# Performance work log

Hardware: AMD Instinct MI355X
Metric: run time of the kernel (lower is better)

The kernel has to match this reference:

```python
import jax, jax.numpy as jnp
import numpy as np

B, N, D, H = 8, 1024, 768, 12
HD = D // H
SCALE = HD ** -0.5

def setup_inputs() -> dict:
    key = jax.random.key(0)
    k1, k2, k3, k4 = jax.random.split(key, 4)
    x = jax.random.normal(k1, (B, N, D), dtype=jnp.float32)
    weight = jax.random.uniform(k2, (B, N), dtype=jnp.float32)
    W_qkv = jax.random.normal(k3, (D, 3 * D), dtype=jnp.float32) * (D ** -0.5)
    W_msa = jax.random.normal(k4, (D, D), dtype=jnp.float32) * (D ** -0.5)
    b_msa = jnp.zeros((D,), dtype=jnp.float32)
    return {"x": x, "weight": weight, "W_qkv": W_qkv, "W_msa": W_msa, "b_msa": b_msa}

def reference(x, weight, W_qkv, W_msa, b_msa):
    # QKV projection (no bias), then elementwise per-token gate
    qkv = jnp.einsum('bnd,de->bne', x, W_qkv)          # [B,N,3D]
    qkv = weight[:, :, None] * qkv
    qkv = qkv.reshape(B, N, 3, H, HD).transpose(2, 0, 3, 1, 4)  # [3,B,H,N,hd]
    q, k, v = qkv[0], qkv[1], qkv[2]
    A = jnp.einsum('bhnd,bhmd->bhnm', q, k) * SCALE    # [B,H,N,N]
    A = jax.nn.softmax(A, axis=-1)
    out = jnp.einsum('bhnm,bhmd->bhnd', A, v)          # [B,H,N,hd]
    out = out.transpose(0, 2, 1, 3).reshape(B, N, D)
    return jnp.einsum('bnd,de->bne', out, W_msa) + b_msa
```

## Files before the change

### kernel.cpp

```cpp
#include <hip/hip_runtime.h>
#include <hip/hip_bf16.h>


typedef __attribute__((ext_vector_type(8))) short bf8;
typedef __attribute__((ext_vector_type(4))) float f4;

#define QSCALE 0.1803368801111204f

static __device__ __forceinline__ short bf16_of(float f) {
    union { float f; unsigned u; } a; a.f = f;
    unsigned r = a.u + 0x7FFFu + ((a.u >> 16) & 1u);
    return (short)(r >> 16);
}

static __device__ __forceinline__ unsigned bfpk(float lo, float hi) {
    float2 t; t.x = lo; t.y = hi;
    __hip_bfloat162 b = __float22bfloat162_rn(t);
    union { __hip_bfloat162 b; unsigned u; } c; c.b = b;
    return c.u;
}

static __device__ __forceinline__ void async16(const short* g, short* l) {
    __builtin_amdgcn_global_load_lds(
        (const __attribute__((address_space(1))) void*)g,
        (__attribute__((address_space(3))) void*)l, 16, 0, 0);
}

static __device__ __forceinline__ void transpose64(
        const float* __restrict__ w, short* __restrict__ wt,
        int K, int E, int k0, int e0, int tid, short (*t)[65]) {
#pragma unroll
    for (int p = 0; p < 16; ++p) {
        int idx = p * 256 + tid;
        int r = idx >> 6, c = idx & 63;
        t[r][c] = bf16_of(w[(k0 + r) * E + e0 + c]);
    }
    __syncthreads();
#pragma unroll
    for (int p = 0; p < 16; ++p) {
        int idx = p * 256 + tid;
        int r = idx >> 6, c = idx & 63;
        wt[(e0 + r) * K + k0 + c] = t[c][r];
    }
}

__global__ __launch_bounds__(256) void k_prep(
        const float* __restrict__ x, const float* __restrict__ gate,
        short* __restrict__ xb,
        const float* __restrict__ Wqkv, short* __restrict__ wtq,
        const float* __restrict__ Wmsa, short* __restrict__ wtm) {
    __shared__ short t[64][65];
    const int bid = blockIdx.x, tid = threadIdx.x;
    if (bid < 3072) {
        int i = bid * 256 + tid;
        const float g = gate[i / 96];
        const f4* sp = (const f4*)x;
        f4 a = sp[2 * i], b = sp[2 * i + 1];
        union { bf8 v; short h[8]; } o;
        o.h[0] = bf16_of(a[0] * g); o.h[1] = bf16_of(a[1] * g);
        o.h[2] = bf16_of(a[2] * g); o.h[3] = bf16_of(a[3] * g);
        o.h[4] = bf16_of(b[0] * g); o.h[5] = bf16_of(b[1] * g);
        o.h[6] = bf16_of(b[2] * g); o.h[7] = bf16_of(b[3] * g);
        ((bf8*)xb)[i] = o.v;
    } else if (bid < 3504) {
        int tt = bid - 3072;
        transpose64(Wqkv, wtq, 768, 2304, (tt / 36) * 64, (tt % 36) * 64, tid, t);
    } else {
        int tt = bid - 3504;
        transpose64(Wmsa, wtm, 768, 768, (tt / 12) * 64, (tt % 12) * 64, tid, t);
    }
}

static __device__ __forceinline__ void gemm128(const short* __restrict__ gA,
                                               const short* __restrict__ gB,
                                               short* smem,
                                               f4 acc[4][4]) {
    const int tid = threadIdx.x, lane = tid & 63;
    const int l16 = lane & 15, quad = lane >> 4, rx = l16 & 7;
    const int wm = (tid >> 6) & 1, wn = tid >> 7;

    auto stage = [&](short* S, int k0) {
#pragma unroll
        for (int c = 0; c < 4; ++c) {
            int p = c * 256 + tid;
            int row = p >> 3, slot = p & 7;
            int gc = slot ^ (row & 7);
            async16(gA + row * 768 + k0 + gc * 8, S + p * 8);
            async16(gB + row * 768 + k0 + gc * 8, S + 8192 + p * 8);
        }
    };

    stage(smem, 0);
    for (int it = 0; it < 12; ++it) {
        __builtin_amdgcn_s_waitcnt(0);
        __syncthreads();
        short* Sc = smem + (it & 1) * 16384;
        if (it + 1 < 12) stage(smem + ((it + 1) & 1) * 16384, (it + 1) * 64);
        const short* As = Sc;
        const short* Bs = Sc + 8192;
#pragma unroll
        for (int ks = 0; ks < 2; ++ks) {
            bf8 af[4], bfr[4];
#pragma unroll
            for (int mt = 0; mt < 4; ++mt)
                af[mt] = *(const bf8*)(As + (wm * 64 + mt * 16 + l16) * 64 +
                                       (((ks * 4 + quad) ^ rx) * 8));
#pragma unroll
            for (int nt = 0; nt < 4; ++nt)
                bfr[nt] = *(const bf8*)(Bs + (wn * 64 + nt * 16 + l16) * 64 +
                                        (((ks * 4 + quad) ^ rx) * 8));
#pragma unroll
            for (int mt = 0; mt < 4; ++mt)
#pragma unroll
                for (int nt = 0; nt < 4; ++nt)
                    acc[mt][nt] = __builtin_amdgcn_mfma_f32_16x16x32_bf16(
                        af[mt], bfr[nt], acc[mt][nt], 0, 0, 0);
        }
    }
    __syncthreads();
}

__global__ __launch_bounds__(512, 2) void k_gemm_qkv(
        const short* __restrict__ xb, const short* __restrict__ wtq,
        short* __restrict__ qb, short* __restrict__ kb, short* __restrict__ vt) {
    __shared__ short lds[69632];
    const int tid = threadIdx.x, lane = tid & 63;
    const int l16 = lane & 15, quad = lane >> 4, rx = l16 & 7;
    const int wv = tid >> 6, wm = wv >> 1, wn = wv & 1;

    const int wg = blockIdx.x;
    const int swz = (wg & 7) * 32 + (wg >> 3);
    const int mI = swz >> 3, nI = swz & 7;
    const int m0 = mI * 256, n0 = nI * 288;

    const short* gA = xb + m0 * 768;
    const short* gB = wtq + n0 * 768;

    auto stageA = [&](int buf, int half, int k0) {
        short* dst = lds + buf * 34816 + half * 8192;
        const short* src = gA + half * 98304 + k0;
#pragma unroll
        for (int j = 0; j < 2; ++j) {
            int p = j * 512 + tid;
            int row = p >> 3;
            int gc = (p & 7) ^ (row & 7);
            async16(src + row * 768 + gc * 8, dst + p * 8);
        }
    };
    auto stageB = [&](int buf, int half, int k0) {
        short* dst = lds + buf * 34816 + 16384 + half * 9216;
        const short* src = gB + half * 110592 + k0;
#pragma unroll
        for (int j = 0; j < 2; ++j) {
            int p = j * 512 + tid;
            int row = p >> 3;
            int gc = (p & 7) ^ (row & 7);
            async16(src + row * 768 + gc * 8, dst + p * 8);
        }
        if (tid < 128) {
            int p = 1024 + tid;
            int row = p >> 3;
            int gc = (p & 7) ^ (row & 7);
            async16(src + row * 768 + gc * 8, dst + p * 8);
        }
    };

    f4 z = {0.f, 0.f, 0.f, 0.f};
    f4 acc[4][9];
#pragma unroll
    for (int mf = 0; mf < 4; ++mf)
#pragma unroll
        for (int nf = 0; nf < 9; ++nf) acc[mf][nf] = z;

    stageA(0, 0, 0); stageA(0, 1, 0);
    stageB(0, 0, 0); stageB(0, 1, 0);
    stageB(1, 0, 64);
    if (wv < 2) asm volatile("s_waitcnt vmcnt(3)" ::: "memory");
    else        asm volatile("s_waitcnt vmcnt(2)" ::: "memory");
    __builtin_amdgcn_s_barrier();

#pragma unroll 2
    for (int t = 0; t < 12; ++t) {
        const short* Ab = lds + (t & 1) * 34816;
        const short* Bb = Ab + 16384;
        auto rdA = [&](int mf, int ks) {
            return *(const bf8*)(Ab + (wm * 64 + mf * 16 + l16) * 64 +
                                 (((ks * 4 + quad) ^ rx) << 3));
        };
        auto rdB = [&](int nf, int ks) {
            return *(const bf8*)(Bb + (wn * 144 + nf * 16 + l16) * 64 +
                                 (((ks * 4 + quad) ^ rx) << 3));
        };
        bf8 af01[2][2], af23[2][2], bfr[5][2];

#pragma unroll
        for (int mf = 0; mf < 2; ++mf) { af01[mf][0] = rdA(mf, 0); af01[mf][1] = rdA(mf, 1); }
#pragma unroll
        for (int nf = 0; nf < 5; ++nf) { bfr[nf][0] = rdB(nf, 0); bfr[nf][1] = rdB(nf, 1); }
        if (t < 11) stageB((t + 1) & 1, 1, (t + 1) * 64);
        __builtin_amdgcn_s_barrier();
        __builtin_amdgcn_s_setprio(1);
#pragma unroll
        for (int mf = 0; mf < 2; ++mf)
#pragma unroll
            for (int nf = 0; nf < 5; ++nf) {
                acc[mf][nf] = __builtin_amdgcn_mfma_f32_16x16x32_bf16(
                    af01[mf][0], bfr[nf][0], acc[mf][nf], 0, 0, 0);
                acc[mf][nf] = __builtin_amdgcn_mfma_f32_16x16x32_bf16(
                    af01[mf][1], bfr[nf][1], acc[mf][nf], 0, 0, 0);
            }
        __builtin_amdgcn_s_setprio(0);
        __builtin_amdgcn_s_barrier();

#pragma unroll
        for (int mf = 0; mf < 2; ++mf) { af23[mf][0] = rdA(mf + 2, 0); af23[mf][1] = rdA(mf + 2, 1); }
        if (t < 11) stageA((t + 1) & 1, 0, (t + 1) * 64);
        __builtin_amdgcn_s_barrier();
        __builtin_amdgcn_s_setprio(1);
#pragma unroll
        for (int mf = 0; mf < 2; ++mf)
#pragma unroll
            for (int nf = 0; nf < 5; ++nf) {
                acc[mf + 2][nf] = __builtin_amdgcn_mfma_f32_16x16x32_bf16(
                    af23[mf][0], bfr[nf][0], acc[mf + 2][nf], 0, 0, 0);
                acc[mf + 2][nf] = __builtin_amdgcn_mfma_f32_16x16x32_bf16(
                    af23[mf][1], bfr[nf][1], acc[mf + 2][nf], 0, 0, 0);
            }
        __builtin_amdgcn_s_setprio(0);
        __builtin_amdgcn_s_barrier();

        bf8 bfh[4][2];
#pragma unroll
        for (int nf = 0; nf < 4; ++nf) { bfh[nf][0] = rdB(nf + 5, 0); bfh[nf][1] = rdB(nf + 5, 1); }
        if (t < 11) stageA((t + 1) & 1, 1, (t + 1) * 64);
        __builtin_amdgcn_s_barrier();
        __builtin_amdgcn_s_setprio(1);
#pragma unroll
        for (int mf = 0; mf < 2; ++mf)
#pragma unroll
            for (int nf = 0; nf < 4; ++nf) {
                acc[mf + 2][nf + 5] = __builtin_amdgcn_mfma_f32_16x16x32_bf16(
                    af23[mf][0], bfh[nf][0], acc[mf + 2][nf + 5], 0, 0, 0);
                acc[mf + 2][nf + 5] = __builtin_amdgcn_mfma_f32_16x16x32_bf16(
                    af23[mf][1], bfh[nf][1], acc[mf + 2][nf + 5], 0, 0, 0);
            }
        __builtin_amdgcn_s_setprio(0);
        __builtin_amdgcn_s_barrier();

#pragma unroll
        for (int mf = 0; mf < 2; ++mf) { af01[mf][0] = rdA(mf, 0); af01[mf][1] = rdA(mf, 1); }
        if (t < 10) stageB(t & 1, 0, (t + 2) * 64);
        __builtin_amdgcn_s_barrier();
        __builtin_amdgcn_s_setprio(1);
#pragma unroll
        for (int mf = 0; mf < 2; ++mf)
#pragma unroll
            for (int nf = 0; nf < 4; ++nf) {
                acc[mf][nf + 5] = __builtin_amdgcn_mfma_f32_16x16x32_bf16(
                    af01[mf][0], bfh[nf][0], acc[mf][nf + 5], 0, 0, 0);
                acc[mf][nf + 5] = __builtin_amdgcn_mfma_f32_16x16x32_bf16(
                    af01[mf][1], bfh[nf][1], acc[mf][nf + 5], 0, 0, 0);
            }
        __builtin_amdgcn_s_setprio(0);
        if (t < 10) {
            if (wv < 2) asm volatile("s_waitcnt vmcnt(3)" ::: "memory");
            else        asm volatile("s_waitcnt vmcnt(2)" ::: "memory");
        } else if (t == 10) {
            asm volatile("s_waitcnt vmcnt(0)" ::: "memory");
        }
        __builtin_amdgcn_s_barrier();
    }

    const int bI = m0 >> 10, nn0 = m0 & 1023;
#pragma unroll
    for (int nf = 0; nf < 9; ++nf) {
        const int ct = n0 + wn * 144 + nf * 16;
        if (ct < 1536) {
            const int which = (ct >= 768) ? 1 : 0;
            const int h = (ct - which * 768) >> 6;
            const int hd = (ct & 63) + l16;
            short* dst = (which ? kb : qb) + (bI * 12 + h) * 65536 + hd;
#pragma unroll
            for (int mf = 0; mf < 4; ++mf)
#pragma unroll
                for (int r = 0; r < 4; ++r) {
                    const int nn = nn0 + wm * 64 + mf * 16 + quad * 4 + r;
                    const float val = acc[mf][nf][r];
                    dst[nn * 64] = bf16_of(which ? val : val * QSCALE);
                }
        }
    }
    const int vstart = (n0 >= 1536) ? n0 : 1536;
    const int npass = (n0 + 288 > vstart) ? (n0 + 288 - vstart) / 96 : 0;
    for (int p = 0; p < npass; ++p) {
        __syncthreads();
        const int c0 = vstart + p * 96;
#pragma unroll
        for (int nf = 0; nf < 9; ++nf) {
            const int ct = n0 + wn * 144 + nf * 16;
            if (ct >= c0 && ct < c0 + 96) {
                const int lc = ct - c0 + l16;
#pragma unroll
                for (int mf = 0; mf < 4; ++mf)
#pragma unroll
                    for (int r = 0; r < 4; ++r) {
                        const int rl = wm * 64 + mf * 16 + quad * 4 + r;
                        lds[lc * 264 + rl] = bf16_of(acc[mf][nf][r]);
                    }
            }
        }
        __syncthreads();
        const int vg0 = c0 - 1536;
#pragma unroll
        for (int u = 0; u < 6; ++u) {
            const int idx = u * 512 + tid;
            const int lc = idx >> 5, ck = idx & 31;
            const int vg = vg0 + lc;
            const int h = vg >> 6, hd = vg & 63;
            bf8 vv = *(const bf8*)(lds + lc * 264 + ck * 8);
            *(bf8*)(vt + ((bI * 12 + h) * 64 + hd) * 1024 + nn0 + ck * 8) = vv;
        }
    }
}

__global__ __launch_bounds__(256) void k_gemm_final(
        const short* __restrict__ attn, const short* __restrict__ wtm,
        const float* __restrict__ bias, float* __restrict__ out) {
    __shared__ short smem[32768];
    const int lane = threadIdx.x & 63;
    const int l16 = lane & 15, quad = lane >> 4;
    const int wm = (threadIdx.x >> 6) & 1, wn = threadIdx.x >> 7;
    const int m0 = blockIdx.y * 128, n0 = blockIdx.x * 128;
    f4 z = {0.f, 0.f, 0.f, 0.f};
    f4 acc[4][4] = {{z,z,z,z},{z,z,z,z},{z,z,z,z},{z,z,z,z}};
    gemm128(attn + m0 * 768, wtm + n0 * 768, smem, acc);
#pragma unroll
    for (int mt = 0; mt < 4; ++mt) {
#pragma unroll
        for (int r = 0; r < 4; ++r) {
            const int row = m0 + wm * 64 + mt * 16 + quad * 4 + r;
#pragma unroll
            for (int nt = 0; nt < 4; ++nt) {
                const int e = n0 + wn * 64 + nt * 16 + l16;
                out[row * 768 + e] = acc[mt][nt][r] + bias[e];
            }
        }
    }
}

__global__ __launch_bounds__(256, 3) void k_attn(const short* __restrict__ qb,
                                                 const short* __restrict__ kb,
                                                 const short* __restrict__ vt,
                                                 short* __restrict__ attn) {
    __shared__ short Ks[2][4096];
    __shared__ short Vs[2][4096];
    const int tid = threadIdx.x, wave = tid >> 6, lane = tid & 63;
    const int l16 = lane & 15, quad = lane >> 4;
    const int bh = blockIdx.x;
    const int b = bh / 12, h = bh - b * 12;
    const int m_base = blockIdx.y * 128 + wave * 32;
    const short* qh = qb + bh * 65536;
    const short* kh = kb + bh * 65536;
    const short* vh = vt + bh * 65536;

    const int rA = ((l16 >> 2) << 3) + (l16 & 3);
    const int fK = (((rA >> 3) & 1) << 2) + (rA & 3);
    const int sK = (quad ^ fK) * 8;
    const int oAlo = rA * 64 + sK;
    const int oAhi = rA * 64 + (sK ^ 32);
    const int oBlo = oAlo + 256, oBhi = oAhi + 256;
    const int fV = (((l16 >> 3) & 1) << 2) + (l16 & 3);
    const int oV = l16 * 64 + ((quad ^ fV) * 8);

    const short* qp0 = qh + (m_base + l16) * 64 + quad * 8;
    bf8 qf00 = *(const bf8*)(qp0);
    bf8 qf01 = *(const bf8*)(qp0 + 32);
    const short* qp1 = qp0 + 16 * 64;
    bf8 qf10 = *(const bf8*)(qp1);
    bf8 qf11 = *(const bf8*)(qp1 + 32);

    union { bf8 v; short h[8]; } onef;
#pragma unroll
    for (int i = 0; i < 8; ++i) onef.h[i] = (short)0x3F80;

    f4 z = {0.f, 0.f, 0.f, 0.f};
    f4 acc0[4] = {z, z, z, z};
    f4 acc1[4] = {z, z, z, z};
    f4 accl0 = z, accl1 = z;

    auto stage = [&](int buf, int j0) {
#pragma unroll
        for (int j = 0; j < 2; ++j) {
            int idx = j * 256 + tid;
            int row = idx >> 3;
            int fr = (((row >> 3) & 1) << 2) + (row & 3);
            int gc = (idx & 7) ^ fr;
            async16(kh + (j0 + row) * 64 + gc * 8, Ks[buf] + idx * 8);
            async16(vh + row * 1024 + j0 + gc * 8, Vs[buf] + idx * 8);
        }
    };

    stage(0, 0);
    int cur = 0;
    for (int it = 0; it < 16; ++it) {
        __builtin_amdgcn_s_waitcnt(0);
        __syncthreads();
        if (it + 1 < 16) stage(cur ^ 1, (it + 1) * 64);
        const short* Kc = Ks[cur];
        const short* Vc = Vs[cur];

#pragma unroll
        for (int jj = 0; jj < 64; jj += 32) {
            const short* kjj = Kc + jj * 64;
            bf8 kAlo = *(const bf8*)(kjj + oAlo);
            bf8 kAhi = *(const bf8*)(kjj + oAhi);
            bf8 kBlo = *(const bf8*)(kjj + oBlo);
            bf8 kBhi = *(const bf8*)(kjj + oBhi);
            bf8 vf0 = *(const bf8*)(Vc + 0 * 1024 + (oV ^ (jj ? 32 : 0)));
            bf8 vf1 = *(const bf8*)(Vc + 1 * 1024 + (oV ^ (jj ? 32 : 0)));
            bf8 vf2 = *(const bf8*)(Vc + 2 * 1024 + (oV ^ (jj ? 32 : 0)));
            bf8 vf3 = *(const bf8*)(Vc + 3 * 1024 + (oV ^ (jj ? 32 : 0)));

            {
                f4 sA = z, sB = z;
                sA = __builtin_amdgcn_mfma_f32_16x16x32_bf16(kAlo, qf00, sA, 0, 0, 0);
                sA = __builtin_amdgcn_mfma_f32_16x16x32_bf16(kAhi, qf01, sA, 0, 0, 0);
                sB = __builtin_amdgcn_mfma_f32_16x16x32_bf16(kBlo, qf00, sB, 0, 0, 0);
                sB = __builtin_amdgcn_mfma_f32_16x16x32_bf16(kBhi, qf01, sB, 0, 0, 0);
                float a0 = __builtin_amdgcn_exp2f(sA[0]);
                float a1 = __builtin_amdgcn_exp2f(sA[1]);
                float a2 = __builtin_amdgcn_exp2f(sA[2]);
                float a3 = __builtin_amdgcn_exp2f(sA[3]);
                float b0 = __builtin_amdgcn_exp2f(sB[0]);
                float b1 = __builtin_amdgcn_exp2f(sB[1]);
                float b2 = __builtin_amdgcn_exp2f(sB[2]);
                float b3 = __builtin_amdgcn_exp2f(sB[3]);
                union { bf8 v; unsigned u[4]; } p;
                p.u[0] = bfpk(a0, a1); p.u[1] = bfpk(a2, a3);
                p.u[2] = bfpk(b0, b1); p.u[3] = bfpk(b2, b3);
                accl0 = __builtin_amdgcn_mfma_f32_16x16x32_bf16(
                    onef.v, p.v, accl0, 0, 0, 0);
                acc0[0] = __builtin_amdgcn_mfma_f32_16x16x32_bf16(vf0, p.v, acc0[0], 0, 0, 0);
                acc0[1] = __builtin_amdgcn_mfma_f32_16x16x32_bf16(vf1, p.v, acc0[1], 0, 0, 0);
                acc0[2] = __builtin_amdgcn_mfma_f32_16x16x32_bf16(vf2, p.v, acc0[2], 0, 0, 0);
                acc0[3] = __builtin_amdgcn_mfma_f32_16x16x32_bf16(vf3, p.v, acc0[3], 0, 0, 0);
            }
            {
                f4 sA = z, sB = z;
                sA = __builtin_amdgcn_mfma_f32_16x16x32_bf16(kAlo, qf10, sA, 0, 0, 0);
                sA = __builtin_amdgcn_mfma_f32_16x16x32_bf16(kAhi, qf11, sA, 0, 0, 0);
                sB = __builtin_amdgcn_mfma_f32_16x16x32_bf16(kBlo, qf10, sB, 0, 0, 0);
                sB = __builtin_amdgcn_mfma_f32_16x16x32_bf16(kBhi, qf11, sB, 0, 0, 0);
                float a0 = __builtin_amdgcn_exp2f(sA[0]);
                float a1 = __builtin_amdgcn_exp2f(sA[1]);
                float a2 = __builtin_amdgcn_exp2f(sA[2]);
                float a3 = __builtin_amdgcn_exp2f(sA[3]);
                float b0 = __builtin_amdgcn_exp2f(sB[0]);
                float b1 = __builtin_amdgcn_exp2f(sB[1]);
                float b2 = __builtin_amdgcn_exp2f(sB[2]);
                float b3 = __builtin_amdgcn_exp2f(sB[3]);
                union { bf8 v; unsigned u[4]; } p;
                p.u[0] = bfpk(a0, a1); p.u[1] = bfpk(a2, a3);
                p.u[2] = bfpk(b0, b1); p.u[3] = bfpk(b2, b3);
                accl1 = __builtin_amdgcn_mfma_f32_16x16x32_bf16(
                    onef.v, p.v, accl1, 0, 0, 0);
                acc1[0] = __builtin_amdgcn_mfma_f32_16x16x32_bf16(vf0, p.v, acc1[0], 0, 0, 0);
                acc1[1] = __builtin_amdgcn_mfma_f32_16x16x32_bf16(vf1, p.v, acc1[1], 0, 0, 0);
                acc1[2] = __builtin_amdgcn_mfma_f32_16x16x32_bf16(vf2, p.v, acc1[2], 0, 0, 0);
                acc1[3] = __builtin_amdgcn_mfma_f32_16x16x32_bf16(vf3, p.v, acc1[3], 0, 0, 0);
            }
        }
        cur ^= 1;
    }

    const float inv0 = 1.f / accl0[0];
    const float inv1 = 1.f / accl1[0];
    const int row0 = (b << 10) + m_base + l16;
    short* op0 = attn + row0 * 768 + h * 64 + quad * 4;
    short* op1 = op0 + 16 * 768;
#pragma unroll
    for (int dt = 0; dt < 4; ++dt)
#pragma unroll
        for (int r = 0; r < 4; ++r) {
            op0[dt * 16 + r] = bf16_of(acc0[dt][r] * inv0);
            op1[dt * 16 + r] = bf16_of(acc1[dt][r] * inv1);
        }
}

extern "C" void kernel_launch(void* const* d_in, const int* in_sizes, int n_in,
                              void* d_out, int out_size, void* d_ws, size_t ws_size,
                              hipStream_t stream) {
    const float* x    = (const float*)d_in[0];
    const float* gate = (const float*)d_in[1];
    const float* Wqkv = (const float*)d_in[2];
    const float* Wmsa = (const float*)d_in[3];
    const float* bmsa = (const float*)d_in[4];
    float* out = (float*)d_out;

    char* ws = (char*)d_ws;
    short* xb  = (short*)(ws);
    short* wtq = (short*)(ws + 12582912);
    short* wtm = (short*)(ws + 16121856);
    short* qb  = (short*)(ws + 17301504);
    short* kb  = (short*)(ws + 29884416);
    short* vt  = (short*)(ws + 42467328);
    short* attn = xb;

    k_prep<<<3648, 256, 0, stream>>>(x, gate, xb, Wqkv, wtq, Wmsa, wtm);
    k_gemm_qkv<<<256, 512, 0, stream>>>(xb, wtq, qb, kb, vt);
    k_attn<<<dim3(96, 8), 256, 0, stream>>>(qb, kb, vt, attn);
    k_gemm_final<<<dim3(6, 64), 256, 0, stream>>>(attn, wtm, bmsa, out);
}
```

Baseline: 177.8 us.

## Retile QKV GEMM to 128-row tiles with triple-buffered BK=32 pipeline

Rewrites the QKV projection GEMM to use 128x288 tiles instead of 256x288, doubling the grid to 512 blocks. It also replaces the double-buffered BK=64 schedule, which had four barriers per step, with a triple-buffered BK=32 pipeline that prefetches two stages ahead and uses a single barrier per step. LDS use drops so the launch bounds now request 4 blocks per CU, aiming for higher occupancy and better latency hiding. The cost is lower arithmetic intensity per block, more global traffic for the weight tiles, and twice as many k-iterations.

```diff
diff --git a/kernel.cpp b/kernel.cpp
--- a/kernel.cpp
+++ b/kernel.cpp
@@ -6,6 +6,7 @@
 typedef __attribute__((ext_vector_type(4))) float f4;
 
 #define QSCALE 0.1803368801111204f
+#define MFMA16 __builtin_amdgcn_mfma_f32_16x16x32_bf16
 
 static __device__ __forceinline__ short bf16_of(float f) {
     union { float f; unsigned u; } a; a.f = f;
@@ -113,159 +114,101 @@
             for (int mt = 0; mt < 4; ++mt)
 #pragma unroll
                 for (int nt = 0; nt < 4; ++nt)
-                    acc[mt][nt] = __builtin_amdgcn_mfma_f32_16x16x32_bf16(
-                        af[mt], bfr[nt], acc[mt][nt], 0, 0, 0);
+                    acc[mt][nt] = MFMA16(af[mt], bfr[nt], acc[mt][nt], 0, 0, 0);
         }
     }
     __syncthreads();
 }
 
-__global__ __launch_bounds__(512, 2) void k_gemm_qkv(
+__global__ __launch_bounds__(512, 4) void k_gemm_qkv(
         const short* __restrict__ xb, const short* __restrict__ wtq,
         short* __restrict__ qb, short* __restrict__ kb, short* __restrict__ vt) {
-    __shared__ short lds[69632];
+    __shared__ short lds[39936];
     const int tid = threadIdx.x, lane = tid & 63;
-    const int l16 = lane & 15, quad = lane >> 4, rx = l16 & 7;
+    const int l16 = lane & 15, quad = lane >> 4;
     const int wv = tid >> 6, wm = wv >> 1, wn = wv & 1;
 
     const int wg = blockIdx.x;
-    const int swz = (wg & 7) * 32 + (wg >> 3);
+    const int swz = (wg & 7) * 64 + (wg >> 3);
     const int mI = swz >> 3, nI = swz & 7;
-    const int m0 = mI * 256, n0 = nI * 288;
+    const int m0 = mI * 128, n0 = nI * 288;
 
     const short* gA = xb + m0 * 768;
     const short* gB = wtq + n0 * 768;
 
-    auto stageA = [&](int buf, int half, int k0) {
-        short* dst = lds + buf * 34816 + half * 8192;
-        const short* src = gA + half * 98304 + k0;
+    auto stage = [&](int buf, int k0) {
+        short* base = lds + buf * 13312;
+        {
+            int p = tid, row = p >> 2;
+            int g = (p & 3) ^ ((row >> 1) & 3);
+            async16(gA + row * 768 + k0 + g * 8, base + p * 8);
+        }
 #pragma unroll
         for (int j = 0; j < 2; ++j) {
-            int p = j * 512 + tid;
-            int row = p >> 3;
-            int gc = (p & 7) ^ (row & 7);
-            async16(src + row * 768 + gc * 8, dst + p * 8);
+            int p = j * 512 + tid, row = p >> 2;
+            int g = (p & 3) ^ ((row >> 1) & 3);
+            async16(gB + row * 768 + k0 + g * 8, base + 4096 + p * 8);
+        }
+        if (tid < 128) {
+            int p = 1024 + tid, row = p >> 2;
+            int g = (p & 3) ^ ((row >> 1) & 3);
+            async16(gB + row * 768 + k0 + g * 8, base + 4096 + p * 8);
         }
     };
-    auto stageB = [&](int buf, int half, int k0) {
-        short* dst = lds + buf * 34816 + 16384 + half * 9216;
-        const short* src = gB + half * 110592 + k0;
-#pragma unroll
-        for (int j = 0; j < 2; ++j) {
-            int p = j * 512 + tid;
-            int row = p >> 3;
-            int gc = (p & 7) ^ (row & 7);
-            async16(src + row * 768 + gc * 8, dst + p * 8);
-        }
-        if (tid < 128) {
-            int p = 1024 + tid;
-            int row = p >> 3;
-            int gc = (p & 7) ^ (row & 7);
-            async16(src + row * 768 + gc * 8, dst + p * 8);
-        }
+
+    auto rdA = [&](const short* base, int mf) {
+        int row = wm * 32 + mf * 16 + l16;
+        int c = row * 4 + (quad ^ ((row >> 1) & 3));
+        return *(const bf8*)(base + c * 8);
     };
+    auto rdB = [&](const short* base, int nf) {
+        int row = wn * 144 + nf * 16 + l16;
+        int c = row * 4 + (quad ^ ((row >> 1) & 3));
+        return *(const bf8*)(base + 4096 + c * 8);
+    };
 
     f4 z = {0.f, 0.f, 0.f, 0.f};
-    f4 acc[4][9];
-#pragma unroll
-    for (int mf = 0; mf < 4; ++mf)
+    f4 acc[2][9];
+#pragma unroll
+    for (int mf = 0; mf < 2; ++mf)
 #pragma unroll
         for (int nf = 0; nf < 9; ++nf) acc[mf][nf] = z;
 
-    stageA(0, 0, 0); stageA(0, 1, 0);
-    stageB(0, 0, 0); stageB(0, 1, 0);
-    stageB(1, 0, 64);
-    if (wv < 2) asm volatile("s_waitcnt vmcnt(3)" ::: "memory");
-    else        asm volatile("s_waitcnt vmcnt(2)" ::: "memory");
+    stage(0, 0); stage(1, 32);
+    if (wv < 2) asm volatile("s_waitcnt vmcnt(4)" ::: "memory");
+    else        asm volatile("s_waitcnt vmcnt(3)" ::: "memory");
     __builtin_amdgcn_s_barrier();
 
-#pragma unroll 2
-    for (int t = 0; t < 12; ++t) {
-        const short* Ab = lds + (t & 1) * 34816;
-        const short* Bb = Ab + 16384;
-        auto rdA = [&](int mf, int ks) {
-            return *(const bf8*)(Ab + (wm * 64 + mf * 16 + l16) * 64 +
-                                 (((ks * 4 + quad) ^ rx) << 3));
-        };
-        auto rdB = [&](int nf, int ks) {
-            return *(const bf8*)(Bb + (wn * 144 + nf * 16 + l16) * 64 +
-                                 (((ks * 4 + quad) ^ rx) << 3));
-        };
-        bf8 af01[2][2], af23[2][2], bfr[5][2];
-
-#pragma unroll
-        for (int mf = 0; mf < 2; ++mf) { af01[mf][0] = rdA(mf, 0); af01[mf][1] = rdA(mf, 1); }
-#pragma unroll
-        for (int nf = 0; nf < 5; ++nf) { bfr[nf][0] = rdB(nf, 0); bfr[nf][1] = rdB(nf, 1); }
-        if (t < 11) stageB((t + 1) & 1, 1, (t + 1) * 64);
-        __builtin_amdgcn_s_barrier();
+#pragma unroll 3
+    for (int t = 0; t < 24; ++t) {
+        const short* cur = lds + (t % 3) * 13312;
+        bf8 af[2];
+        af[0] = rdA(cur, 0); af[1] = rdA(cur, 1);
+        bf8 bfr[5];
+#pragma unroll
+        for (int nf = 0; nf < 5; ++nf) bfr[nf] = rdB(cur, nf);
+        if (t < 22) stage((t + 2) % 3, (t + 2) * 32);
         __builtin_amdgcn_s_setprio(1);
 #pragma unroll
         for (int mf = 0; mf < 2; ++mf)
 #pragma unroll
-            for (int nf = 0; nf < 5; ++nf) {
-                acc[mf][nf] = __builtin_amdgcn_mfma_f32_16x16x32_bf16(
-                    af01[mf][0], bfr[nf][0], acc[mf][nf], 0, 0, 0);
-                acc[mf][nf] = __builtin_amdgcn_mfma_f32_16x16x32_bf16(
-                    af01[mf][1], bfr[nf][1], acc[mf][nf], 0, 0, 0);
-            }
+            for (int nf = 0; nf < 5; ++nf)
+                acc[mf][nf] = MFMA16(af[mf], bfr[nf], acc[mf][nf], 0, 0, 0);
         __builtin_amdgcn_s_setprio(0);
-        __builtin_amdgcn_s_barrier();
-
-#pragma unroll
-        for (int mf = 0; mf < 2; ++mf) { af23[mf][0] = rdA(mf + 2, 0); af23[mf][1] = rdA(mf + 2, 1); }
-        if (t < 11) stageA((t + 1) & 1, 0, (t + 1) * 64);
-        __builtin_amdgcn_s_barrier();
+        bf8 bfh[4];
+#pragma unroll
+        for (int nf = 0; nf < 4; ++nf) bfh[nf] = rdB(cur, nf + 5);
         __builtin_amdgcn_s_setprio(1);
 #pragma unroll
         for (int mf = 0; mf < 2; ++mf)
 #pragma unroll
-            for (int nf = 0; nf < 5; ++nf) {
-                acc[mf + 2][nf] = __builtin_amdgcn_mfma_f32_16x16x32_bf16(
-                    af23[mf][0], bfr[nf][0], acc[mf + 2][nf], 0, 0, 0);
-                acc[mf + 2][nf] = __builtin_amdgcn_mfma_f32_16x16x32_bf16(
-                    af23[mf][1], bfr[nf][1], acc[mf + 2][nf], 0, 0, 0);
-            }
+            for (int nf = 0; nf < 4; ++nf)
+                acc[mf][nf + 5] = MFMA16(af[mf], bfh[nf], acc[mf][nf + 5], 0, 0, 0);
         __builtin_amdgcn_s_setprio(0);
-        __builtin_amdgcn_s_barrier();
-
-        bf8 bfh[4][2];
-#pragma unroll
-        for (int nf = 0; nf < 4; ++nf) { bfh[nf][0] = rdB(nf + 5, 0); bfh[nf][1] = rdB(nf + 5, 1); }
-        if (t < 11) stageA((t + 1) & 1, 1, (t + 1) * 64);
-        __builtin_amdgcn_s_barrier();
-        __builtin_amdgcn_s_setprio(1);
-#pragma unroll
-        for (int mf = 0; mf < 2; ++mf)
-#pragma unroll
-            for (int nf = 0; nf < 4; ++nf) {
-                acc[mf + 2][nf + 5] = __builtin_amdgcn_mfma_f32_16x16x32_bf16(
-                    af23[mf][0], bfh[nf][0], acc[mf + 2][nf + 5], 0, 0, 0);
-                acc[mf + 2][nf + 5] = __builtin_amdgcn_mfma_f32_16x16x32_bf16(
-                    af23[mf][1], bfh[nf][1], acc[mf + 2][nf + 5], 0, 0, 0);
-            }
-        __builtin_amdgcn_s_setprio(0);
-        __builtin_amdgcn_s_barrier();
-
-#pragma unroll
-        for (int mf = 0; mf < 2; ++mf) { af01[mf][0] = rdA(mf, 0); af01[mf][1] = rdA(mf, 1); }
-        if (t < 10) stageB(t & 1, 0, (t + 2) * 64);
-        __builtin_amdgcn_s_barrier();
-        __builtin_amdgcn_s_setprio(1);
-#pragma unroll
-        for (int mf = 0; mf < 2; ++mf)
-#pragma unroll
-            for (int nf = 0; nf < 4; ++nf) {
-                acc[mf][nf + 5] = __builtin_amdgcn_mfma_f32_16x16x32_bf16(
-                    af01[mf][0], bfh[nf][0], acc[mf][nf + 5], 0, 0, 0);
-                acc[mf][nf + 5] = __builtin_amdgcn_mfma_f32_16x16x32_bf16(
-                    af01[mf][1], bfh[nf][1], acc[mf][nf + 5], 0, 0, 0);
-            }
-        __builtin_amdgcn_s_setprio(0);
-        if (t < 10) {
-            if (wv < 2) asm volatile("s_waitcnt vmcnt(3)" ::: "memory");
-            else        asm volatile("s_waitcnt vmcnt(2)" ::: "memory");
-        } else if (t == 10) {
+        if (t < 22) {
+            if (wv < 2) asm volatile("s_waitcnt vmcnt(4)" ::: "memory");
+            else        asm volatile("s_waitcnt vmcnt(3)" ::: "memory");
+        } else if (t == 22) {
             asm volatile("s_waitcnt vmcnt(0)" ::: "memory");
         }
         __builtin_amdgcn_s_barrier();
@@ -281,10 +224,10 @@
             const int hd = (ct & 63) + l16;
             short* dst = (which ? kb : qb) + (bI * 12 + h) * 65536 + hd;
 #pragma unroll
-            for (int mf = 0; mf < 4; ++mf)
+            for (int mf = 0; mf < 2; ++mf)
 #pragma unroll
                 for (int r = 0; r < 4; ++r) {
-                    const int nn = nn0 + wm * 64 + mf * 16 + quad * 4 + r;
+                    const int nn = nn0 + wm * 32 + mf * 16 + quad * 4 + r;
                     const float val = acc[mf][nf][r];
                     dst[nn * 64] = bf16_of(which ? val : val * QSCALE);
                 }
@@ -301,23 +244,23 @@
             if (ct >= c0 && ct < c0 + 96) {
                 const int lc = ct - c0 + l16;
 #pragma unroll
-                for (int mf = 0; mf < 4; ++mf)
+                for (int mf = 0; mf < 2; ++mf)
 #pragma unroll
                     for (int r = 0; r < 4; ++r) {
-                        const int rl = wm * 64 + mf * 16 + quad * 4 + r;
-                        lds[lc * 264 + rl] = bf16_of(acc[mf][nf][r]);
+                        const int rl = wm * 32 + mf * 16 + quad * 4 + r;
+                        lds[lc * 136 + rl] = bf16_of(acc[mf][nf][r]);
                     }
             }
         }
         __syncthreads();
         const int vg0 = c0 - 1536;
 #pragma unroll
-        for (int u = 0; u < 6; ++u) {
+        for (int u = 0; u < 3; ++u) {
             const int idx = u * 512 + tid;
-            const int lc = idx >> 5, ck = idx & 31;
+            const int lc = idx >> 4, ck = idx & 15;
             const int vg = vg0 + lc;
             const int h = vg >> 6, hd = vg & 63;
-            bf8 vv = *(const bf8*)(lds + lc * 264 + ck * 8);
+            bf8 vv = *(const bf8*)(lds + lc * 136 + ck * 8);
             *(bf8*)(vt + ((bI * 12 + h) * 64 + hd) * 1024 + nn0 + ck * 8) = vv;
         }
     }
@@ -423,10 +366,10 @@
 
             {
                 f4 sA = z, sB = z;
-                sA = __builtin_amdgcn_mfma_f32_16x16x32_bf16(kAlo, qf00, sA, 0, 0, 0);
-                sA = __builtin_amdgcn_mfma_f32_16x16x32_bf16(kAhi, qf01, sA, 0, 0, 0);
-                sB = __builtin_amdgcn_mfma_f32_16x16x32_bf16(kBlo, qf00, sB, 0, 0, 0);
-                sB = __builtin_amdgcn_mfma_f32_16x16x32_bf16(kBhi, qf01, sB, 0, 0, 0);
+                sA = MFMA16(kAlo, qf00, sA, 0, 0, 0);
+                sA = MFMA16(kAhi, qf01, sA, 0, 0, 0);
+                sB = MFMA16(kBlo, qf00, sB, 0, 0, 0);
+                sB = MFMA16(kBhi, qf01, sB, 0, 0, 0);
                 float a0 = __builtin_amdgcn_exp2f(sA[0]);
                 float a1 = __builtin_amdgcn_exp2f(sA[1]);
                 float a2 = __builtin_amdgcn_exp2f(sA[2]);
@@ -438,19 +381,18 @@
                 union { bf8 v; unsigned u[4]; } p;
                 p.u[0] = bfpk(a0, a1); p.u[1] = bfpk(a2, a3);
                 p.u[2] = bfpk(b0, b1); p.u[3] = bfpk(b2, b3);
-                accl0 = __builtin_amdgcn_mfma_f32_16x16x32_bf16(
-                    onef.v, p.v, accl0, 0, 0, 0);
-                acc0[0] = __builtin_amdgcn_mfma_f32_16x16x32_bf16(vf0, p.v, acc0[0], 0, 0, 0);
-                acc0[1] = __builtin_amdgcn_mfma_f32_16x16x32_bf16(vf1, p.v, acc0[1], 0, 0, 0);
-                acc0[2] = __builtin_amdgcn_mfma_f32_16x16x32_bf16(vf2, p.v, acc0[2], 0, 0, 0);
-                acc0[3] = __builtin_amdgcn_mfma_f32_16x16x32_bf16(vf3, p.v, acc0[3], 0, 0, 0);
+                accl0 = MFMA16(onef.v, p.v, accl0, 0, 0, 0);
+                acc0[0] = MFMA16(vf0, p.v, acc0[0], 0, 0, 0);
+                acc0[1] = MFMA16(vf1, p.v, acc0[1], 0, 0, 0);
+                acc0[2] = MFMA16(vf2, p.v, acc0[2], 0, 0, 0);
+                acc0[3] = MFMA16(vf3, p.v, acc0[3], 0, 0, 0);
             }
             {
                 f4 sA = z, sB = z;
-                sA = __builtin_amdgcn_mfma_f32_16x16x32_bf16(kAlo, qf10, sA, 0, 0, 0);
-                sA = __builtin_amdgcn_mfma_f32_16x16x32_bf16(kAhi, qf11, sA, 0, 0, 0);
-                sB = __builtin_amdgcn_mfma_f32_16x16x32_bf16(kBlo, qf10, sB, 0, 0, 0);
-                sB = __builtin_amdgcn_mfma_f32_16x16x32_bf16(kBhi, qf11, sB, 0, 0, 0);
+                sA = MFMA16(kAlo, qf10, sA, 0, 0, 0);
+                sA = MFMA16(kAhi, qf11, sA, 0, 0, 0);
+                sB = MFMA16(kBlo, qf10, sB, 0, 0, 0);
+                sB = MFMA16(kBhi, qf11, sB, 0, 0, 0);
                 float a0 = __builtin_amdgcn_exp2f(sA[0]);
                 float a1 = __builtin_amdgcn_exp2f(sA[1]);
                 float a2 = __builtin_amdgcn_exp2f(sA[2]);
@@ -462,12 +404,11 @@
                 union { bf8 v; unsigned u[4]; } p;
                 p.u[0] = bfpk(a0, a1); p.u[1] = bfpk(a2, a3);
                 p.u[2] = bfpk(b0, b1); p.u[3] = bfpk(b2, b3);
-                accl1 = __builtin_amdgcn_mfma_f32_16x16x32_bf16(
-                    onef.v, p.v, accl1, 0, 0, 0);
-                acc1[0] = __builtin_amdgcn_mfma_f32_16x16x32_bf16(vf0, p.v, acc1[0], 0, 0, 0);
-                acc1[1] = __builtin_amdgcn_mfma_f32_16x16x32_bf16(vf1, p.v, acc1[1], 0, 0, 0);
-                acc1[2] = __builtin_amdgcn_mfma_f32_16x16x32_bf16(vf2, p.v, acc1[2], 0, 0, 0);
-                acc1[3] = __builtin_amdgcn_mfma_f32_16x16x32_bf16(vf3, p.v, acc1[3], 0, 0, 0);
+                accl1 = MFMA16(onef.v, p.v, accl1, 0, 0, 0);
+                acc1[0] = MFMA16(vf0, p.v, acc1[0], 0, 0, 0);
+                acc1[1] = MFMA16(vf1, p.v, acc1[1], 0, 0, 0);
+                acc1[2] = MFMA16(vf2, p.v, acc1[2], 0, 0, 0);
+                acc1[3] = MFMA16(vf3, p.v, acc1[3], 0, 0, 0);
             }
         }
         cur ^= 1;
@@ -507,7 +448,7 @@
     short* attn = xb;
 
     k_prep<<<3648, 256, 0, stream>>>(x, gate, xb, Wqkv, wtq, Wmsa, wtm);
-    k_gemm_qkv<<<256, 512, 0, stream>>>(xb, wtq, qb, kb, vt);
+    k_gemm_qkv<<<512, 512, 0, stream>>>(xb, wtq, qb, kb, vt);
     k_attn<<<dim3(96, 8), 256, 0, stream>>>(qb, kb, vt, attn);
     k_gemm_final<<<dim3(6, 64), 256, 0, stream>>>(attn, wtm, bmsa, out);
 }
```

Measured after the change: 211.3 us. +18.9%, slower.
